# Kernel optimization log

Hardware: AMD Instinct MI355X
Metric: run time of the kernel (lower is better)

## Reference

```python
import jax, jax.numpy as jnp
import numpy as np

T, B_SZ = 1024, 1024
NX, NU, ND, NM, NDT, NH = 128, 64, 32, 32, 32, 128


def setup_inputs() -> dict:
    key = jax.random.key(0)
    ks = jax.random.split(key, 10)
    return {
        "x": jax.random.normal(ks[0], (B_SZ, NX), jnp.float32),
        "M_flow": jax.random.normal(ks[1], (T, B_SZ, NM), jnp.float32),
        "DT": jax.random.normal(ks[2], (T, B_SZ, NDT), jnp.float32),
        "D": jax.random.normal(ks[3], (T, B_SZ, ND), jnp.float32),
        # ConstrainedLinear(nx, nx): weight and scalar init with torch.rand -> uniform[0,1)
        "A_weight": jax.random.uniform(ks[4], (NX, NX), jnp.float32),
        "A_scalar": jax.random.uniform(ks[5], (NX, NX), jnp.float32),
        # nn.Linear(in, out, bias=False) weights are [out, in]
        "B_w": jax.random.normal(ks[6], (NX, NU), jnp.float32) * (1.0 / np.sqrt(NU)),
        "E_w": jax.random.normal(ks[7], (NX, ND), jnp.float32) * (1.0 / np.sqrt(ND)),
        "hf1_w": jax.random.normal(ks[8], (NH, NM + NDT), jnp.float32) * (1.0 / np.sqrt(NM + NDT)),
        "hf2_w": jax.random.normal(ks[9], (NU, NH), jnp.float32) * (1.0 / np.sqrt(NH)),
    }


def reference(x, M_flow, DT, D, A_weight, A_scalar, B_w, E_w, hf1_w, hf2_w):
    # Constrained weight: ((1 - 0.1*sigmoid(scalar)) * softmax(weight, dim=1)).T
    # It is constant across time, so compute once (torch redundantly recomputes it per step).
    s_clamped = 1.0 - 0.1 * jax.nn.sigmoid(A_scalar)
    W_eff = (s_clamped * jax.nn.softmax(A_weight, axis=1)).T  # [nx, nx]

    # Per-step control input u_t depends only on exogenous M_flow/DT -> vectorize over time.
    md = jnp.concatenate([M_flow, DT], axis=2)                # [T, B, n_m+n_dT]
    h = jax.nn.relu(jnp.einsum('tbi,hi->tbh', md, hf1_w))     # [T, B, n_hidden]
    u = jax.nn.relu(jnp.einsum('tbh,uh->tbu', h, hf2_w))      # [T, B, nu]

    # Precompute additive drive B(u_t) + E(d_t); only x@W_eff is sequential.
    drive = jnp.einsum('tbu,xu->tbx', u, B_w) + jnp.einsum('tbd,xd->tbx', D, E_w)

    def step(x_prev, drive_t):
        x_new = x_prev @ W_eff + drive_t
        return x_new, x_new

    _, X = jax.lax.scan(step, x, drive)  # X: [T, B, nx]
    Y = X[:, :, -1]                      # [T, B]
    return X, Y
```

## Files before the change

kernel.cpp:

```cpp
#include <hip/hip_runtime.h>

typedef _Float16 h4 __attribute__((ext_vector_type(4)));
typedef _Float16 h8 __attribute__((ext_vector_type(8)));
typedef float f4 __attribute__((ext_vector_type(4)));

#define MFMA16(a, b, c) __builtin_amdgcn_mfma_f32_16x16x32_f16((a), (b), (c), 0, 0, 0)

static constexpr int TT  = 1024;
static constexpr int BS  = 1024;
static constexpr int LCH = 32;
static constexpr int NCH = 32;
static constexpr size_t XTOT = (size_t)TT * BS * 128;

static constexpr size_t WS_WT16 = 0;
static constexpr size_t WS_HF1  = 32768;
static constexpr size_t WS_HF2  = 49152;
static constexpr size_t WS_BW   = 65536;
static constexpr size_t WS_EW   = 81920;
static constexpr size_t WS_W32  = 90112;
static constexpr size_t WS_F    = 131072;
static constexpr size_t WS_INIT = WS_F + (size_t)NCH * BS * 128 * 4;
static constexpr size_t WS_DRV  = WS_INIT + (size_t)NCH * BS * 128 * 4;

template <typename T>
__device__ inline T ntload(const T* p) { return __builtin_nontemporal_load(p); }

__global__ void prep_kernel(const float* __restrict__ Aw, const float* __restrict__ As,
                            const float* __restrict__ hf1, const float* __restrict__ hf2,
                            const float* __restrict__ Bw, const float* __restrict__ Ew,
                            char* __restrict__ ws)
{
    const int tid = threadIdx.x;
    const int bid = blockIdx.x;
    if (bid < 128) {
        __shared__ float red[128];
        const int n = bid;
        const float a = Aw[n * 128 + tid];
        red[tid] = a;
        __syncthreads();
        for (int s = 64; s > 0; s >>= 1) {
            if (tid < s) red[tid] = fmaxf(red[tid], red[tid + s]);
            __syncthreads();
        }
        const float mx = red[0];
        __syncthreads();
        const float e = expf(a - mx);
        red[tid] = e;
        __syncthreads();
        for (int s = 64; s > 0; s >>= 1) {
            if (tid < s) red[tid] += red[tid + s];
            __syncthreads();
        }
        const float sm  = e / red[0];
        const float asv = As[n * 128 + tid];
        const float sc  = 1.0f - 0.1f * (1.0f / (1.0f + expf(-asv)));
        ((_Float16*)(ws + WS_WT16))[n * 128 + tid] = (_Float16)(sc * sm);
    } else {
        const int b2 = bid - 128;
        for (int i = b2 * 128 + tid; i < 8192; i += 32 * 128) {
            ((_Float16*)(ws + WS_HF1))[i] = (_Float16)hf1[i];
            ((_Float16*)(ws + WS_HF2))[i] = (_Float16)hf2[i];
            ((_Float16*)(ws + WS_BW))[i]  = (_Float16)Bw[i];
            if (i < 4096) ((_Float16*)(ws + WS_EW))[i] = (_Float16)Ew[i];
        }
    }
}

__global__ void w32_kernel(char* __restrict__ ws)
{
    const int tid  = threadIdx.x;
    const int lane = tid & 63;
    const int w    = tid >> 6;
    const int cl   = lane & 15;
    const int gq   = lane >> 4;

    __shared__ __align__(16) _Float16 Ta[128 * 128];
    __shared__ __align__(16) _Float16 Tb[128 * 128];

    const _Float16* Wt16 = (const _Float16*)(ws + WS_WT16);
    for (int i = tid; i < 2048; i += 256)
        *(h8*)&Ta[i * 8] = *(const h8*)&Wt16[i * 8];
    __syncthreads();

    for (int s = 0; s < 5; ++s) {
        const _Float16* src = (s & 1) ? Tb : Ta;
        _Float16* dst       = (s & 1) ? Ta : Tb;
        f4 acc[8][2];
#pragma unroll
        for (int mt = 0; mt < 8; ++mt)
#pragma unroll
            for (int nt = 0; nt < 2; ++nt) acc[mt][nt] = f4{};
#pragma unroll
        for (int kk = 0; kk < 4; ++kk) {
            h8 b0, b1;
#pragma unroll
            for (int j = 0; j < 8; ++j) {
                const int kr = kk * 32 + gq * 8 + j;
                b0[j] = src[kr * 128 + w * 32 + cl];
                b1[j] = src[kr * 128 + w * 32 + 16 + cl];
            }
#pragma unroll
            for (int mt = 0; mt < 8; ++mt) {
                h8 a = *(const h8*)&src[(mt * 16 + cl) * 128 + kk * 32 + gq * 8];
                acc[mt][0] = MFMA16(a, b0, acc[mt][0]);
                acc[mt][1] = MFMA16(a, b1, acc[mt][1]);
            }
        }
        __syncthreads();
#pragma unroll
        for (int mt = 0; mt < 8; ++mt)
#pragma unroll
            for (int nt = 0; nt < 2; ++nt)
#pragma unroll
                for (int r = 0; r < 4; ++r)
                    dst[(mt * 16 + gq * 4 + r) * 128 + w * 32 + nt * 16 + cl] =
                        (_Float16)acc[mt][nt][r];
        __syncthreads();
    }
    _Float16* W32 = (_Float16*)(ws + WS_W32);
    for (int i = tid; i < 2048; i += 256)
        *(h8*)&W32[i * 8] = *(const h8*)&Tb[i * 8];
}

__global__ __launch_bounds__(256, 4)
void drive_kernel(const float* __restrict__ Mfl, const float* __restrict__ DTi,
                  const float* __restrict__ Din, char* __restrict__ ws, int t0)
{
    const int tid  = threadIdx.x;
    const int lane = tid & 63;
    const int w    = tid >> 6;
    const int cl   = lane & 15;
    const int gq   = lane >> 4;
    const int bt   = blockIdx.x & 63;
    const int tq   = blockIdx.x >> 6;
    const int b0   = bt * 16;

    const _Float16* Hf1  = (const _Float16*)(ws + WS_HF1);
    const _Float16* Hf2  = (const _Float16*)(ws + WS_HF2);
    const _Float16* Bw16 = (const _Float16*)(ws + WS_BW);
    const _Float16* Ew16 = (const _Float16*)(ws + WS_EW);
    _Float16* Drv        = (_Float16*)(ws + WS_DRV);

    __shared__ __align__(16) _Float16 mds[4][16 * 64];
    __shared__ __align__(16) _Float16 dts[4][16 * 32];
    __shared__ __align__(16) _Float16 hs[4][16 * 128];
    __shared__ __align__(16) _Float16 us[4][16 * 64];

    const int qrow = (tid & 127) >> 3;
    const int qc4  = (tid & 7) * 4;
    f4 pm[4], pd[4];
#pragma unroll
    for (int s = 0; s < 4; ++s) {
        const size_t t  = (size_t)(t0 + tq * 4 + s);
        const size_t rb = (t * BS + b0 + qrow) * 32 + qc4;
        pm[s] = (tid < 128) ? ntload((const f4*)&Mfl[rb]) : ntload((const f4*)&DTi[rb]);
        if (tid < 128) pd[s] = ntload((const f4*)&Din[rb]);
    }
#pragma unroll
    for (int s = 0; s < 4; ++s) {
        const int col = (tid < 128) ? qc4 : (32 + qc4);
        h4 hv;
#pragma unroll
        for (int j = 0; j < 4; ++j) hv[j] = (_Float16)pm[s][j];
        *(h4*)&mds[s][qrow * 64 + (((col >> 3) ^ (qrow & 7)) * 8) + (col & 7)] = hv;
        if (tid < 128) {
            h4 h2;
#pragma unroll
            for (int j = 0; j < 4; ++j) h2[j] = (_Float16)pd[s][j];
            *(h4*)&dts[s][qrow * 32 + (((qc4 >> 3) ^ (qrow & 3)) * 8) + (qc4 & 7)] = h2;
        }
    }

    h8 hf1f[2][2], bwf[2][2], ewf[2], hf2f[4];
#pragma unroll
    for (int nt = 0; nt < 2; ++nt) {
        const int ng = w * 32 + nt * 16 + cl;
#pragma unroll
        for (int kk = 0; kk < 2; ++kk) {
            hf1f[nt][kk] = *(const h8*)&Hf1[ng * 64 + kk * 32 + gq * 8];
            bwf[nt][kk]  = *(const h8*)&Bw16[ng * 64 + kk * 32 + gq * 8];
        }
        ewf[nt] = *(const h8*)&Ew16[ng * 32 + gq * 8];
    }
    {
        const int ng = w * 16 + cl;
#pragma unroll
        for (int kk = 0; kk < 4; ++kk)
            hf2f[kk] = *(const h8*)&Hf2[ng * 128 + kk * 32 + gq * 8];
    }
    __syncthreads();

#pragma unroll
    for (int s = 0; s < 4; ++s) {
        f4 ha[2] = {};
#pragma unroll
        for (int kk = 0; kk < 2; ++kk) {
            h8 a = *(const h8*)&mds[s][cl * 64 + (((kk * 4 + gq) ^ (cl & 7)) * 8)];
            ha[0] = MFMA16(a, hf1f[0][kk], ha[0]);
            ha[1] = MFMA16(a, hf1f[1][kk], ha[1]);
        }
#pragma unroll
        for (int nt = 0; nt < 2; ++nt) {
            const int colg = w * 32 + nt * 16 + cl;
#pragma unroll
            for (int r = 0; r < 4; ++r) {
                const int row = gq * 4 + r;
                hs[s][row * 128 + (((colg >> 3) ^ (row & 15)) * 8) + (colg & 7)] =
                    (_Float16)fmaxf(ha[nt][r], 0.f);
            }
        }
    }
    __syncthreads();

#pragma unroll
    for (int s = 0; s < 4; ++s) {
        f4 ua = {};
#pragma unroll
        for (int kk = 0; kk < 4; ++kk) {
            h8 a = *(const h8*)&hs[s][cl * 128 + (((kk * 4 + gq) ^ (cl & 15)) * 8)];
            ua = MFMA16(a, hf2f[kk], ua);
        }
        const int colg = w * 16 + cl;
#pragma unroll
        for (int r = 0; r < 4; ++r) {
            const int row = gq * 4 + r;
            us[s][row * 64 + (((colg >> 3) ^ (row & 7)) * 8) + (colg & 7)] =
                (_Float16)fmaxf(ua[r], 0.f);
        }
    }
    __syncthreads();

#pragma unroll
    for (int s = 0; s < 4; ++s) {
        f4 acc[2] = {};
#pragma unroll
        for (int kk = 0; kk < 2; ++kk) {
            h8 a = *(const h8*)&us[s][cl * 64 + (((kk * 4 + gq) ^ (cl & 7)) * 8)];
            acc[0] = MFMA16(a, bwf[0][kk], acc[0]);
            acc[1] = MFMA16(a, bwf[1][kk], acc[1]);
        }
        {
            h8 a = *(const h8*)&dts[s][cl * 32 + ((gq ^ (cl & 3)) * 8)];
            acc[0] = MFMA16(a, ewf[0], acc[0]);
            acc[1] = MFMA16(a, ewf[1], acc[1]);
        }
#pragma unroll
        for (int nt = 0; nt < 2; ++nt) {
            const int n = w * 32 + nt * 16 + cl;
#pragma unroll
            for (int r = 0; r < 4; ++r) {
                const int b = gq * 4 + r;
                hs[s][b * 128 + (((n >> 3) ^ b) & 15) * 8 + (n & 7)] = (_Float16)acc[nt][r];
            }
        }
    }
    __syncthreads();

    {
        const int s2 = tid >> 6;
        const int l2 = tid & 63, c2 = l2 & 15, g2 = l2 >> 4;
        const size_t tl = (size_t)tq * 4 + s2;
        _Float16* dst = &Drv[(((size_t)tl * 64 + bt) * 64 + l2) * 32];
#pragma unroll
        for (int p = 0; p < 4; ++p) {
            h4 lo = *(const h4*)&hs[s2][c2 * 128 + (((4 * p + (g2 >> 1)) ^ c2) & 15) * 8 + (g2 & 1) * 4];
            h4 hi = *(const h4*)&hs[s2][c2 * 128 + (((4 * p + 2 + (g2 >> 1)) ^ c2) & 15) * 8 + (g2 & 1) * 4];
            h8 o;
#pragma unroll
            for (int j = 0; j < 4; ++j) { o[j] = lo[j]; o[4 + j] = hi[j]; }
            *(h8*)&dst[p * 8] = o;
        }
    }
}

template <bool FINAL>
__global__ __launch_bounds__(128, 1)
void scan_kernel(char* __restrict__ ws, int c0,
                 float* __restrict__ Xout, float* __restrict__ Yout)
{
    const int wslot = threadIdx.x >> 6;
    const int wid   = blockIdx.x * 2 + wslot;
    const int lane  = threadIdx.x & 63;
    const int cl = lane & 15, gq = lane >> 4;
    const int c  = c0 + (wid >> 6);
    const int bt = wid & 63;
    const int b0 = bt * 16;
    const int cloc = c & 15;

    const _Float16* Wt16 = (const _Float16*)(ws + WS_WT16);
    const _Float16* Drv  = (const _Float16*)(ws + WS_DRV);
    float* Fbuf       = (float*)(ws + WS_F);
    const float* Init = (const float*)(ws + WS_INIT);

    __shared__ __align__(16) _Float16 tb[2][16 * 128];
    _Float16* tbuf = tb[wslot];

    h8 wf[8][4];
#pragma unroll
    for (int nt = 0; nt < 8; ++nt)
#pragma unroll
        for (int kt = 0; kt < 4; ++kt)
            wf[nt][kt] = *(const h8*)&Wt16[(nt * 16 + cl) * 128 + kt * 32 + gq * 8];

    h8 xf[4];
    if constexpr (FINAL) {
        f4 iv[8];
#pragma unroll
        for (int nt = 0; nt < 8; ++nt)
            iv[nt] = *(const f4*)&Init[((size_t)c * BS + b0 + cl) * 128 + nt * 16 + gq * 4];
#pragma unroll
        for (int nt = 0; nt < 8; ++nt) {
            h4 hv;
#pragma unroll
            for (int r = 0; r < 4; ++r) hv[r] = (_Float16)iv[nt][r];
            *(h4*)&tbuf[cl * 128 + (((nt * 2 + (gq >> 1)) ^ cl) & 15) * 8 + (gq & 1) * 4] = hv;
        }
#pragma unroll
        for (int kt = 0; kt < 4; ++kt)
            xf[kt] = *(const h8*)&tbuf[cl * 128 + (((kt * 4 + gq) ^ cl) & 15) * 8];
    } else {
#pragma unroll
        for (int kt = 0; kt < 4; ++kt) xf[kt] = h8{};
    }

    const h8* dp = (const h8*)&Drv[(((size_t)cloc * 32 * 64 + bt) * 64 + lane) * 32];
    h8 dr[4];
#pragma unroll
    for (int p = 0; p < 4; ++p) dr[p] = dp[p];

    for (int k = 0; k < LCH; ++k) {
        f4 acc[8];
#pragma unroll
        for (int p = 0; p < 4; ++p)
#pragma unroll
            for (int r = 0; r < 4; ++r) {
                acc[2 * p][r]     = (float)dr[p][r];
                acc[2 * p + 1][r] = (float)dr[p][4 + r];
            }
        if (k + 1 < LCH) {
            const h8* np = dp + (size_t)(k + 1) * 16384;
#pragma unroll
            for (int p = 0; p < 4; ++p) dr[p] = np[p];
        }
#pragma unroll
        for (int kt = 0; kt < 4; ++kt)
#pragma unroll
            for (int nt = 0; nt < 8; ++nt)
                acc[nt] = MFMA16(wf[nt][kt], xf[kt], acc[nt]);

        if constexpr (FINAL) {
            const size_t t = (size_t)c * LCH + k;
            float* xp = &Xout[(t * BS + b0 + cl) * 128 + gq * 4];
#pragma unroll
            for (int nt = 0; nt < 8; ++nt)
                __builtin_nontemporal_store(acc[nt], (f4*)&xp[nt * 16]);
            if (gq == 3)
                __builtin_nontemporal_store(acc[7][3], &Yout[t * BS + b0 + cl]);
        } else if (k == LCH - 1) {
#pragma unroll
            for (int nt = 0; nt < 8; ++nt)
                *(f4*)&Fbuf[((size_t)c * BS + b0 + cl) * 128 + nt * 16 + gq * 4] = acc[nt];
        }
        if (k < LCH - 1) {
#pragma unroll
            for (int nt = 0; nt < 8; ++nt) {
                h4 hv;
#pragma unroll
                for (int r = 0; r < 4; ++r) hv[r] = (_Float16)acc[nt][r];
                *(h4*)&tbuf[cl * 128 + (((nt * 2 + (gq >> 1)) ^ cl) & 15) * 8 + (gq & 1) * 4] = hv;
            }
#pragma unroll
            for (int kt = 0; kt < 4; ++kt)
                xf[kt] = *(const h8*)&tbuf[cl * 128 + (((kt * 4 + gq) ^ cl) & 15) * 8];
        }
    }
}

__global__ __launch_bounds__(64, 1)
void carry_kernel(const float* __restrict__ x0, char* __restrict__ ws,
                  int cc_lo, int n_steps, int copy0)
{
    const int lane = threadIdx.x;
    const int cl = lane & 15, gq = lane >> 4;
    const int b0 = blockIdx.x * 16;

    const _Float16* W32 = (const _Float16*)(ws + WS_W32);
    const float* Fbuf   = (const float*)(ws + WS_F);
    float* Init         = (float*)(ws + WS_INIT);

    __shared__ __align__(16) _Float16 tbuf[16 * 128];

    h8 wf[8][4];
#pragma unroll
    for (int nt = 0; nt < 8; ++nt)
#pragma unroll
        for (int kt = 0; kt < 4; ++kt)
            wf[nt][kt] = *(const h8*)&W32[(nt * 16 + cl) * 128 + kt * 32 + gq * 8];

    h8 xf[4];
    {
        f4 iv[8];
#pragma unroll
        for (int nt = 0; nt < 8; ++nt)
            iv[nt] = *(const f4*)&x0[(size_t)(b0 + cl) * 128 + nt * 16 + gq * 4];
        if (copy0) {
#pragma unroll
            for (int nt = 0; nt < 8; ++nt)
                *(f4*)&Init[((size_t)cc_lo * BS + b0 + cl) * 128 + nt * 16 + gq * 4] = iv[nt];
        }
#pragma unroll
        for (int nt = 0; nt < 8; ++nt) {
            h4 hv;
#pragma unroll
            for (int r = 0; r < 4; ++r) hv[r] = (_Float16)iv[nt][r];
            *(h4*)&tbuf[cl * 128 + (((nt * 2 + (gq >> 1)) ^ cl) & 15) * 8 + (gq & 1) * 4] = hv;
        }
#pragma unroll
        for (int kt = 0; kt < 4; ++kt)
            xf[kt] = *(const h8*)&tbuf[cl * 128 + (((kt * 4 + gq) ^ cl) & 15) * 8];
    }

    for (int i = 1; i <= n_steps; ++i) {
        const int cc = cc_lo + i;
        f4 acc[8];
#pragma unroll
        for (int nt = 0; nt < 8; ++nt)
            acc[nt] = *(const f4*)&Fbuf[((size_t)(cc - 1) * BS + b0 + cl) * 128 + nt * 16 + gq * 4];
#pragma unroll
        for (int kt = 0; kt < 4; ++kt)
#pragma unroll
            for (int nt = 0; nt < 8; ++nt)
                acc[nt] = MFMA16(wf[nt][kt], xf[kt], acc[nt]);
#pragma unroll
        for (int nt = 0; nt < 8; ++nt)
            *(f4*)&Init[((size_t)cc * BS + b0 + cl) * 128 + nt * 16 + gq * 4] = acc[nt];
        if (i < n_steps) {
#pragma unroll
            for (int nt = 0; nt < 8; ++nt) {
                h4 hv;
#pragma unroll
                for (int r = 0; r < 4; ++r) hv[r] = (_Float16)acc[nt][r];
                *(h4*)&tbuf[cl * 128 + (((nt * 2 + (gq >> 1)) ^ cl) & 15) * 8 + (gq & 1) * 4] = hv;
            }
#pragma unroll
            for (int kt = 0; kt < 4; ++kt)
                xf[kt] = *(const h8*)&tbuf[cl * 128 + (((kt * 4 + gq) ^ cl) & 15) * 8];
        }
    }
}

extern "C" void kernel_launch(void* const* d_in, const int* in_sizes, int n_in,
                              void* d_out, int out_size, void* d_ws, size_t ws_size,
                              hipStream_t stream)
{
    const float* x_in = (const float*)d_in[0];
    const float* Mfl  = (const float*)d_in[1];
    const float* DTi  = (const float*)d_in[2];
    const float* Din  = (const float*)d_in[3];
    const float* Aw   = (const float*)d_in[4];
    const float* As   = (const float*)d_in[5];
    const float* Bw   = (const float*)d_in[6];
    const float* Ew   = (const float*)d_in[7];
    const float* hf1  = (const float*)d_in[8];
    const float* hf2  = (const float*)d_in[9];
    char* ws    = (char*)d_ws;
    float* Xout = (float*)d_out;
    float* Yout = Xout + XTOT;
    const float* Init16 = (const float*)(ws + WS_INIT) + (size_t)16 * BS * 128;

    prep_kernel<<<dim3(160), dim3(128), 0, stream>>>(Aw, As, hf1, hf2, Bw, Ew, ws);
    w32_kernel<<<dim3(1), dim3(256), 0, stream>>>(ws);

    drive_kernel<<<dim3(128 * 64), dim3(256), 0, stream>>>(Mfl, DTi, Din, ws, 0);
    scan_kernel<false><<<dim3(512), dim3(128), 0, stream>>>(ws, 0, nullptr, nullptr);
    carry_kernel<<<dim3(64), dim3(64), 0, stream>>>(x_in, ws, 0, 16, 1);
    scan_kernel<true><<<dim3(512), dim3(128), 0, stream>>>(ws, 0, Xout, Yout);

    drive_kernel<<<dim3(128 * 64), dim3(256), 0, stream>>>(Mfl, DTi, Din, ws, 512);
    scan_kernel<false><<<dim3(480), dim3(128), 0, stream>>>(ws, 16, nullptr, nullptr);
    carry_kernel<<<dim3(64), dim3(64), 0, stream>>>(Init16, ws, 16, 15, 0);
    scan_kernel<true><<<dim3(512), dim3(128), 0, stream>>>(ws, 16, Xout, Yout);
}
```

Measured before the change: 502.6 us.

## Run drive and chunked scan over the full sequence in a single pass

The two half-sequence passes are merged into one. The drive kernel now fills drive terms for all 1024 timesteps. One scan launch covers all 32 chunks, followed by a single 31-step carry kernel and one final scan. The scan kernel moves to 4 waves per block and unrolls its time loop by two, prefetching drive values two steps ahead. The aim is to cut launch count and serialization and to expose twice as many independent waves per scan launch. The cost is a drive workspace twice as large, which must fit in the provided buffer, plus higher register pressure from the extra prefetch.

```diff
diff --git a/kernel.cpp b/kernel.cpp
--- a/kernel.cpp
+++ b/kernel.cpp
@@ -124,7 +124,7 @@
 
 __global__ __launch_bounds__(256, 4)
 void drive_kernel(const float* __restrict__ Mfl, const float* __restrict__ DTi,
-                  const float* __restrict__ Din, char* __restrict__ ws, int t0)
+                  const float* __restrict__ Din, char* __restrict__ ws)
 {
     const int tid  = threadIdx.x;
     const int lane = tid & 63;
@@ -151,7 +151,7 @@
     f4 pm[4], pd[4];
 #pragma unroll
     for (int s = 0; s < 4; ++s) {
-        const size_t t  = (size_t)(t0 + tq * 4 + s);
+        const size_t t  = (size_t)tq * 4 + s;
         const size_t rb = (t * BS + b0 + qrow) * 32 + qc4;
         pm[s] = (tid < 128) ? ntload((const f4*)&Mfl[rb]) : ntload((const f4*)&DTi[rb]);
         if (tid < 128) pd[s] = ntload((const f4*)&Din[rb]);
@@ -259,8 +259,8 @@
     {
         const int s2 = tid >> 6;
         const int l2 = tid & 63, c2 = l2 & 15, g2 = l2 >> 4;
-        const size_t tl = (size_t)tq * 4 + s2;
-        _Float16* dst = &Drv[(((size_t)tl * 64 + bt) * 64 + l2) * 32];
+        const size_t t = (size_t)tq * 4 + s2;
+        _Float16* dst = &Drv[(((size_t)t * 64 + bt) * 64 + l2) * 32];
 #pragma unroll
         for (int p = 0; p < 4; ++p) {
             h4 lo = *(const h4*)&hs[s2][c2 * 128 + (((4 * p + (g2 >> 1)) ^ c2) & 15) * 8 + (g2 & 1) * 4];
@@ -274,25 +274,24 @@
 }
 
 template <bool FINAL>
-__global__ __launch_bounds__(128, 1)
-void scan_kernel(char* __restrict__ ws, int c0,
+__global__ __launch_bounds__(256, 2)
+void scan_kernel(char* __restrict__ ws,
                  float* __restrict__ Xout, float* __restrict__ Yout)
 {
     const int wslot = threadIdx.x >> 6;
-    const int wid   = blockIdx.x * 2 + wslot;
+    const int wid   = blockIdx.x * 4 + wslot;
     const int lane  = threadIdx.x & 63;
     const int cl = lane & 15, gq = lane >> 4;
-    const int c  = c0 + (wid >> 6);
+    const int c  = wid >> 6;
     const int bt = wid & 63;
     const int b0 = bt * 16;
-    const int cloc = c & 15;
 
     const _Float16* Wt16 = (const _Float16*)(ws + WS_WT16);
     const _Float16* Drv  = (const _Float16*)(ws + WS_DRV);
     float* Fbuf       = (float*)(ws + WS_F);
     const float* Init = (const float*)(ws + WS_INIT);
 
-    __shared__ __align__(16) _Float16 tb[2][16 * 128];
+    __shared__ __align__(16) _Float16 tb[4][16 * 128];
     _Float16* tbuf = tb[wslot];
 
     h8 wf[8][4];
@@ -323,62 +322,64 @@
         for (int kt = 0; kt < 4; ++kt) xf[kt] = h8{};
     }
 
-    const h8* dp = (const h8*)&Drv[(((size_t)cloc * 32 * 64 + bt) * 64 + lane) * 32];
-    h8 dr[4];
-#pragma unroll
-    for (int p = 0; p < 4; ++p) dr[p] = dp[p];
-
-    for (int k = 0; k < LCH; ++k) {
-        f4 acc[8];
-#pragma unroll
-        for (int p = 0; p < 4; ++p)
-#pragma unroll
-            for (int r = 0; r < 4; ++r) {
-                acc[2 * p][r]     = (float)dr[p][r];
-                acc[2 * p + 1][r] = (float)dr[p][4 + r];
-            }
-        if (k + 1 < LCH) {
-            const h8* np = dp + (size_t)(k + 1) * 16384;
-#pragma unroll
-            for (int p = 0; p < 4; ++p) dr[p] = np[p];
-        }
-#pragma unroll
-        for (int kt = 0; kt < 4; ++kt)
-#pragma unroll
-            for (int nt = 0; nt < 8; ++nt)
-                acc[nt] = MFMA16(wf[nt][kt], xf[kt], acc[nt]);
-
-        if constexpr (FINAL) {
-            const size_t t = (size_t)c * LCH + k;
-            float* xp = &Xout[(t * BS + b0 + cl) * 128 + gq * 4];
-#pragma unroll
-            for (int nt = 0; nt < 8; ++nt)
-                __builtin_nontemporal_store(acc[nt], (f4*)&xp[nt * 16]);
-            if (gq == 3)
-                __builtin_nontemporal_store(acc[7][3], &Yout[t * BS + b0 + cl]);
-        } else if (k == LCH - 1) {
-#pragma unroll
-            for (int nt = 0; nt < 8; ++nt)
-                *(f4*)&Fbuf[((size_t)c * BS + b0 + cl) * 128 + nt * 16 + gq * 4] = acc[nt];
-        }
-        if (k < LCH - 1) {
-#pragma unroll
-            for (int nt = 0; nt < 8; ++nt) {
-                h4 hv;
-#pragma unroll
-                for (int r = 0; r < 4; ++r) hv[r] = (_Float16)acc[nt][r];
-                *(h4*)&tbuf[cl * 128 + (((nt * 2 + (gq >> 1)) ^ cl) & 15) * 8 + (gq & 1) * 4] = hv;
-            }
-#pragma unroll
-            for (int kt = 0; kt < 4; ++kt)
-                xf[kt] = *(const h8*)&tbuf[cl * 128 + (((kt * 4 + gq) ^ cl) & 15) * 8];
-        }
-    }
+    constexpr size_t STEP = 16384;
+    const h8* dp = (const h8*)&Drv[(((size_t)(c * LCH) * 64 + bt) * 64 + lane) * 32];
+    h8 dra0, dra1, dra2, dra3, drb0, drb1, drb2, drb3;
+    dra0 = dp[0]; dra1 = dp[1]; dra2 = dp[2]; dra3 = dp[3];
+    drb0 = dp[STEP + 0]; drb1 = dp[STEP + 1]; drb2 = dp[STEP + 2]; drb3 = dp[STEP + 3];
+
+#define SCAN_STEP(K, D0, D1, D2, D3)                                                     \
+    {                                                                                    \
+        f4 acc[8];                                                                       \
+        _Pragma("unroll") for (int r = 0; r < 4; ++r) {                                  \
+            acc[0][r] = (float)D0[r]; acc[1][r] = (float)D0[4 + r];                      \
+            acc[2][r] = (float)D1[r]; acc[3][r] = (float)D1[4 + r];                      \
+            acc[4][r] = (float)D2[r]; acc[5][r] = (float)D2[4 + r];                      \
+            acc[6][r] = (float)D3[r]; acc[7][r] = (float)D3[4 + r];                      \
+        }                                                                                \
+        if ((K) + 2 < LCH) {                                                             \
+            D0 = dp[(size_t)((K) + 2) * STEP + 0];                                       \
+            D1 = dp[(size_t)((K) + 2) * STEP + 1];                                       \
+            D2 = dp[(size_t)((K) + 2) * STEP + 2];                                       \
+            D3 = dp[(size_t)((K) + 2) * STEP + 3];                                       \
+        }                                                                                \
+        _Pragma("unroll") for (int kt = 0; kt < 4; ++kt)                                 \
+            _Pragma("unroll") for (int nt = 0; nt < 8; ++nt)                             \
+                acc[nt] = MFMA16(wf[nt][kt], xf[kt], acc[nt]);                           \
+        if constexpr (FINAL) {                                                           \
+            const size_t t = (size_t)c * LCH + (K);                                      \
+            float* xp = &Xout[(t * BS + b0 + cl) * 128 + gq * 4];                        \
+            _Pragma("unroll") for (int nt = 0; nt < 8; ++nt)                             \
+                __builtin_nontemporal_store(acc[nt], (f4*)&xp[nt * 16]);                 \
+            if (gq == 3)                                                                 \
+                __builtin_nontemporal_store(acc[7][3], &Yout[t * BS + b0 + cl]);         \
+        } else if ((K) == LCH - 1) {                                                     \
+            _Pragma("unroll") for (int nt = 0; nt < 8; ++nt)                             \
+                *(f4*)&Fbuf[((size_t)c * BS + b0 + cl) * 128 + nt * 16 + gq * 4] =       \
+                    acc[nt];                                                             \
+        }                                                                                \
+        if ((K) < LCH - 1) {                                                             \
+            _Pragma("unroll") for (int nt = 0; nt < 8; ++nt) {                           \
+                h4 hv;                                                                   \
+                _Pragma("unroll") for (int r = 0; r < 4; ++r)                            \
+                    hv[r] = (_Float16)acc[nt][r];                                        \
+                *(h4*)&tbuf[cl * 128 + (((nt * 2 + (gq >> 1)) ^ cl) & 15) * 8 +          \
+                            (gq & 1) * 4] = hv;                                          \
+            }                                                                            \
+            _Pragma("unroll") for (int kt = 0; kt < 4; ++kt)                             \
+                xf[kt] = *(const h8*)&tbuf[cl * 128 + (((kt * 4 + gq) ^ cl) & 15) * 8];  \
+        }                                                                                \
+    }
+
+    for (int k = 0; k < LCH; k += 2) {
+        SCAN_STEP(k, dra0, dra1, dra2, dra3);
+        SCAN_STEP(k + 1, drb0, drb1, drb2, drb3);
+    }
+#undef SCAN_STEP
 }
 
 __global__ __launch_bounds__(64, 1)
-void carry_kernel(const float* __restrict__ x0, char* __restrict__ ws,
-                  int cc_lo, int n_steps, int copy0)
+void carry_kernel(const float* __restrict__ x0, char* __restrict__ ws, int n_steps)
 {
     const int lane = threadIdx.x;
     const int cl = lane & 15, gq = lane >> 4;
@@ -403,11 +404,9 @@
 #pragma unroll
         for (int nt = 0; nt < 8; ++nt)
             iv[nt] = *(const f4*)&x0[(size_t)(b0 + cl) * 128 + nt * 16 + gq * 4];
-        if (copy0) {
-#pragma unroll
-            for (int nt = 0; nt < 8; ++nt)
-                *(f4*)&Init[((size_t)cc_lo * BS + b0 + cl) * 128 + nt * 16 + gq * 4] = iv[nt];
-        }
+#pragma unroll
+        for (int nt = 0; nt < 8; ++nt)
+            *(f4*)&Init[(size_t)(b0 + cl) * 128 + nt * 16 + gq * 4] = iv[nt];
 #pragma unroll
         for (int nt = 0; nt < 8; ++nt) {
             h4 hv;
@@ -420,8 +419,7 @@
             xf[kt] = *(const h8*)&tbuf[cl * 128 + (((kt * 4 + gq) ^ cl) & 15) * 8];
     }
 
-    for (int i = 1; i <= n_steps; ++i) {
-        const int cc = cc_lo + i;
+    for (int cc = 1; cc <= n_steps; ++cc) {
         f4 acc[8];
 #pragma unroll
         for (int nt = 0; nt < 8; ++nt)
@@ -434,7 +432,7 @@
 #pragma unroll
         for (int nt = 0; nt < 8; ++nt)
             *(f4*)&Init[((size_t)cc * BS + b0 + cl) * 128 + nt * 16 + gq * 4] = acc[nt];
-        if (i < n_steps) {
+        if (cc < n_steps) {
 #pragma unroll
             for (int nt = 0; nt < 8; ++nt) {
                 h4 hv;
@@ -466,18 +464,12 @@
     char* ws    = (char*)d_ws;
     float* Xout = (float*)d_out;
     float* Yout = Xout + XTOT;
-    const float* Init16 = (const float*)(ws + WS_INIT) + (size_t)16 * BS * 128;
 
     prep_kernel<<<dim3(160), dim3(128), 0, stream>>>(Aw, As, hf1, hf2, Bw, Ew, ws);
     w32_kernel<<<dim3(1), dim3(256), 0, stream>>>(ws);
 
-    drive_kernel<<<dim3(128 * 64), dim3(256), 0, stream>>>(Mfl, DTi, Din, ws, 0);
-    scan_kernel<false><<<dim3(512), dim3(128), 0, stream>>>(ws, 0, nullptr, nullptr);
-    carry_kernel<<<dim3(64), dim3(64), 0, stream>>>(x_in, ws, 0, 16, 1);
-    scan_kernel<true><<<dim3(512), dim3(128), 0, stream>>>(ws, 0, Xout, Yout);
-
-    drive_kernel<<<dim3(128 * 64), dim3(256), 0, stream>>>(Mfl, DTi, Din, ws, 512);
-    scan_kernel<false><<<dim3(480), dim3(128), 0, stream>>>(ws, 16, nullptr, nullptr);
-    carry_kernel<<<dim3(64), dim3(64), 0, stream>>>(Init16, ws, 16, 15, 0);
-    scan_kernel<true><<<dim3(512), dim3(128), 0, stream>>>(ws, 16, Xout, Yout);
-}
+    drive_kernel<<<dim3(256 * 64), dim3(256), 0, stream>>>(Mfl, DTi, Din, ws);
+    scan_kernel<false><<<dim3(496), dim3(256), 0, stream>>>(ws, nullptr, nullptr);
+    carry_kernel<<<dim3(64), dim3(64), 0, stream>>>(x_in, ws, 31);
+    scan_kernel<true><<<dim3(512), dim3(256), 0, stream>>>(ws, Xout, Yout);
+}
```

New measurement: 482.8 us. 3.9% less time.
